# Performance work log

Measured on AMD Instinct MI355X. Metric: run time of the kernel, lower is better.

The kernel has to match this reference:

```python
import jax, jax.numpy as jnp
import numpy as np

EPS = 1e-7  # keras.backend.epsilon()


def setup_inputs() -> dict:
    key = jax.random.key(0)
    k1, k2, k3 = jax.random.split(key, 3)
    B, N, D_in, C, D_out = 32, 2048, 8, 32, 16
    x = jax.random.normal(k1, (B, N, D_in), dtype=jnp.float32)
    W = jax.random.normal(k2, (1, N, C, D_out, D_in), dtype=jnp.float32) * 0.05
    R = jax.random.normal(k3, (1, N, C), dtype=jnp.float32)
    return {"x": x, "W": W, "R": R}


def reference(x, W, R):
    # x: [B, N, D_in]; W: [1, N, C, D_out, D_in]; R: [1, N, C]
    R_nor = jax.nn.softmax(R[0], axis=0)          # softmax over N (axis=1 of [1,N,C])
    # per-capsule transform: u[b,n,c,j] = sum_k W[n,c,j,k] * x[b,n,k]
    u = jnp.einsum('ncjk,bnk->bncj', W[0], x)
    # routing-weighted aggregation over input capsules n
    s = jnp.einsum('bncj,nc->bcj', u, R_nor)      # [B, C, D_out]
    # squash along capsule dim (original axis=-2 before squeeze == D_out)
    ss = jnp.sum(jnp.square(s), axis=-1, keepdims=True) + EPS
    scale = jnp.sqrt(ss) / (1.0 + ss)
    return scale * s                               # [B, C, D_out]
```

## Files before the change

kernel.cpp:

```cpp
#include <hip/hip_runtime.h>
#include <math.h>


#define NN 2048
#define CC 32

__device__ __forceinline__ void g2l16(const float* g, float* l) {
  __builtin_amdgcn_global_load_lds((const __attribute__((address_space(1))) void*)g,
                                   (__attribute__((address_space(3))) void*)l, 16, 0, 0);
}

__global__ void caps_stats(const float* __restrict__ R, float* __restrict__ I) {
  const int c = blockIdx.x;
  const int t = threadIdx.x;
  __shared__ float red[256];
  float s = 0.f;
#pragma unroll
  for (int i = 0; i < 8; ++i) s += expf(R[(size_t)(t + i * 256) * CC + c]);
  red[t] = s;
  __syncthreads();
  for (int h = 128; h >= 1; h >>= 1) {
    if (t < h) red[t] += red[t + h];
    __syncthreads();
  }
  if (t == 0) I[c] = 1.0f / red[0];
}

__global__ void __launch_bounds__(512) caps_main(const float* __restrict__ x,
                                                 const float* __restrict__ W,
                                                 const float* __restrict__ R,
                                                 const float* __restrict__ I,
                                                 float* __restrict__ P) {
  const int bid = blockIdx.x;
  const int cq = bid >> 6;
  const int chunk = bid & 63;
  const int n0 = chunk * 32;
  const int tid = threadIdx.x;
  const int ws = tid >> 6;
  const int lane = tid & 63;
  const int j = lane & 15;
  const int bo = lane >> 4;

  extern __shared__ float smem[];
  float* ldsW = smem;
  float* ldsX = smem + 8192;
  float* wW = ldsW + ws * 1024;
  float* wX = ldsX + ws * 1024;
  const int nw = n0 + ws * 4;

  auto stageW = [&](int nl, int buf) {
#pragma unroll
    for (int i = 0; i < 2; ++i) {
      int S = i * 64 + lane;
      int g = S ^ (((S >> 2) ^ (S >> 4)) & 1) ^ (((S >> 3) & 1) << 1) ^ (((S >> 4) & 1) << 2);
      g2l16(W + (size_t)(nw + nl) * 4096 + cq * 512 + g * 4, wW + buf * 512 + i * 256);
    }
  };
  stageW(0, 0);
  {
    int g2 = lane ^ ((lane >> 4) << 1);
    int b = g2 >> 1, kq = g2 & 1;
    const float* xs = x + (size_t)b * (NN * 8) + kq * 4;
#pragma unroll
    for (int nl = 0; nl < 4; ++nl)
      g2l16(xs + (size_t)(nw + nl) * 8, wX + nl * 256);
  }
  float rv[4][4];
  {
    float4 iv = *(const float4*)(I + cq * 4);
#pragma unroll
    for (int nl = 0; nl < 4; ++nl) {
      float4 rq = *(const float4*)(R + (size_t)(nw + nl) * CC + cq * 4);
      rv[nl][0] = expf(rq.x) * iv.x;
      rv[nl][1] = expf(rq.y) * iv.y;
      rv[nl][2] = expf(rq.z) * iv.z;
      rv[nl][3] = expf(rq.w) * iv.w;
    }
  }

  float acc[4][8];
#pragma unroll
  for (int a = 0; a < 4; ++a)
#pragma unroll
    for (int b = 0; b < 8; ++b) acc[a][b] = 0.f;

  const int jsw = j >> 1;

  auto compute = [&](int nl, int buf) {
    const float* Wn = wW + buf * 512;
    const float* Xn = wX + nl * 256;
#pragma unroll
    for (int kh = 0; kh < 2; ++kh) {
      float4 xv[8];
#pragma unroll
      for (int bi = 0; bi < 8; ++bi) {
        int G = (bo * 8 + bi) * 2 + kh;
        int S = G ^ ((G >> 4) << 1);
        xv[bi] = *(const float4*)(Xn + S * 4);
      }
#pragma unroll
      for (int ci = 0; ci < 4; ++ci) {
        int slot = (ci * 32 + j * 2 + kh) ^ jsw;
        float4 wf = *(const float4*)(Wn + slot * 4);
        float rvv = rv[nl][ci];
        float w0 = wf.x * rvv, w1 = wf.y * rvv, w2 = wf.z * rvv, w3 = wf.w * rvv;
#pragma unroll
        for (int bi = 0; bi < 8; ++bi) {
          float a = acc[ci][bi];
          a = fmaf(w0, xv[bi].x, a);
          a = fmaf(w1, xv[bi].y, a);
          a = fmaf(w2, xv[bi].z, a);
          a = fmaf(w3, xv[bi].w, a);
          acc[ci][bi] = a;
        }
      }
    }
  };

  stageW(1, 1);
  asm volatile("s_waitcnt vmcnt(2)" ::: "memory");
  __builtin_amdgcn_sched_barrier(0);
  compute(0, 0);
  __builtin_amdgcn_sched_barrier(0);
  stageW(2, 0);
  asm volatile("s_waitcnt vmcnt(2)" ::: "memory");
  __builtin_amdgcn_sched_barrier(0);
  compute(1, 1);
  __builtin_amdgcn_sched_barrier(0);
  stageW(3, 1);
  asm volatile("s_waitcnt vmcnt(2)" ::: "memory");
  __builtin_amdgcn_sched_barrier(0);
  compute(2, 0);
  asm volatile("s_waitcnt vmcnt(0)" ::: "memory");
  __builtin_amdgcn_sched_barrier(0);
  compute(3, 1);

#pragma unroll
  for (int ci = 0; ci < 4; ++ci)
#pragma unroll
    for (int bi = 0; bi < 8; ++bi) {
      int cell = (ci * 8 + bi) * 64 + lane;
      float* dst = (ci < 2) ? (ldsW + ws * 1024 + cell)
                            : (ldsX + ws * 1024 + (cell - 1024));
      *dst = acc[ci][bi];
    }
  __syncthreads();
  {
    const int t4 = tid * 4;
    const bool lo = (t4 < 1024);
    float4 ssum = make_float4(0.f, 0.f, 0.f, 0.f);
#pragma unroll
    for (int w = 0; w < 8; ++w) {
      const float* src = lo ? (ldsW + w * 1024 + t4) : (ldsX + w * 1024 + (t4 - 1024));
      float4 v = *(const float4*)src;
      ssum.x += v.x; ssum.y += v.y; ssum.z += v.z; ssum.w += v.w;
    }
    *(float4*)(P + (size_t)bid * 2048 + t4) = ssum;
  }
}

__global__ void caps_reduce(const float* __restrict__ P, float* __restrict__ out) {
  const int g = blockIdx.x * 256 + threadIdx.x;
  const int j = g & 15;
  const int c = (g >> 4) & 31;
  const int b = g >> 9;
  const int bo = b >> 3, bi = b & 7;
  const int cq = c >> 2, ci = c & 3;
  const int idx = (ci * 8 + bi) * 64 + (bo * 16 + j);
  const float* Pq = P + (size_t)cq * 64 * 2048 + idx;

  float s = 0.f;
#pragma unroll 16
  for (int ch = 0; ch < 64; ++ch) {
    s += Pq[(size_t)ch * 2048];
  }
  float sq = s * s;
  sq += __shfl_xor(sq, 8, 16);
  sq += __shfl_xor(sq, 4, 16);
  sq += __shfl_xor(sq, 2, 16);
  sq += __shfl_xor(sq, 1, 16);
  float ss = sq + 1e-7f;
  float scale = sqrtf(ss) / (1.0f + ss);
  out[g] = scale * s;
}

extern "C" void kernel_launch(void* const* d_in, const int* in_sizes, int n_in,
                              void* d_out, int out_size, void* d_ws, size_t ws_size,
                              hipStream_t stream) {
  const float* x = (const float*)d_in[0];
  const float* W = (const float*)d_in[1];
  const float* R = (const float*)d_in[2];
  float* out = (float*)d_out;

  float* I = (float*)d_ws;
  float* P = (float*)d_ws + 64;

  hipFuncSetAttribute((const void*)caps_main,
                      hipFuncAttributeMaxDynamicSharedMemorySize, 65536);

  caps_stats<<<32, 256, 0, stream>>>(R, I);
  caps_main<<<512, 512, 65536, stream>>>(x, W, R, I, P);
  caps_reduce<<<64, 256, 0, stream>>>(P, out);
}
```

Measured before the change: 26.93 us.

## Process eight capsules per block with triple-buffered W staging

Each block now handles eight output capsules instead of four, which halves the grid to 256 blocks and doubles the per-thread accumulator tile so x values loaded from LDS are reused across more capsules. W staging moves to three LDS buffers with deeper prefetch and adjusted waitcnts, and the R loads are hoisted ahead of the staging. LDS per block grows to 128KB and register pressure roughly doubles, which risks lower occupancy and fewer blocks than CUs.

```diff
diff --git a/kernel.cpp b/kernel.cpp
--- a/kernel.cpp
+++ b/kernel.cpp
@@ -32,7 +32,7 @@
                                                  const float* __restrict__ I,
                                                  float* __restrict__ P) {
   const int bid = blockIdx.x;
-  const int cq = bid >> 6;
+  const int cg = bid >> 6;
   const int chunk = bid & 63;
   const int n0 = chunk * 32;
   const int tid = threadIdx.x;
@@ -42,20 +42,30 @@
   const int bo = lane >> 4;
 
   extern __shared__ float smem[];
-  float* ldsW = smem;
-  float* ldsX = smem + 8192;
-  float* wW = ldsW + ws * 1024;
-  float* wX = ldsX + ws * 1024;
+  float* wREG = smem + ws * 4096;
+  float* wW = wREG;
+  float* wX = wREG + 3072;
   const int nw = n0 + ws * 4;
 
+  float4 iv0 = *(const float4*)(I + cg * 8);
+  float4 iv1 = *(const float4*)(I + cg * 8 + 4);
+  float4 rq0[4], rq1[4];
+#pragma unroll
+  for (int nl = 0; nl < 4; ++nl) {
+    rq0[nl] = *(const float4*)(R + (size_t)(nw + nl) * CC + cg * 8);
+    rq1[nl] = *(const float4*)(R + (size_t)(nw + nl) * CC + cg * 8 + 4);
+  }
+
   auto stageW = [&](int nl, int buf) {
 #pragma unroll
-    for (int i = 0; i < 2; ++i) {
+    for (int i = 0; i < 4; ++i) {
       int S = i * 64 + lane;
-      int g = S ^ (((S >> 2) ^ (S >> 4)) & 1) ^ (((S >> 3) & 1) << 1) ^ (((S >> 4) & 1) << 2);
-      g2l16(W + (size_t)(nw + nl) * 4096 + cq * 512 + g * 4, wW + buf * 512 + i * 256);
+      int g = S ^ ((S >> 3) & 3);
+      g2l16(W + (size_t)(nw + nl) * 4096 + cg * 1024 + g * 4,
+            wW + buf * 1024 + i * 256);
     }
   };
+
   stageW(0, 0);
   {
     int g2 = lane ^ ((lane >> 4) << 1);
@@ -65,29 +75,29 @@
     for (int nl = 0; nl < 4; ++nl)
       g2l16(xs + (size_t)(nw + nl) * 8, wX + nl * 256);
   }
-  float rv[4][4];
-  {
-    float4 iv = *(const float4*)(I + cq * 4);
-#pragma unroll
-    for (int nl = 0; nl < 4; ++nl) {
-      float4 rq = *(const float4*)(R + (size_t)(nw + nl) * CC + cq * 4);
-      rv[nl][0] = expf(rq.x) * iv.x;
-      rv[nl][1] = expf(rq.y) * iv.y;
-      rv[nl][2] = expf(rq.z) * iv.z;
-      rv[nl][3] = expf(rq.w) * iv.w;
-    }
-  }
-
-  float acc[4][8];
-#pragma unroll
-  for (int a = 0; a < 4; ++a)
+  stageW(1, 1);
+
+  float rv[4][8];
+#pragma unroll
+  for (int nl = 0; nl < 4; ++nl) {
+    rv[nl][0] = expf(rq0[nl].x) * iv0.x;
+    rv[nl][1] = expf(rq0[nl].y) * iv0.y;
+    rv[nl][2] = expf(rq0[nl].z) * iv0.z;
+    rv[nl][3] = expf(rq0[nl].w) * iv0.w;
+    rv[nl][4] = expf(rq1[nl].x) * iv1.x;
+    rv[nl][5] = expf(rq1[nl].y) * iv1.y;
+    rv[nl][6] = expf(rq1[nl].z) * iv1.z;
+    rv[nl][7] = expf(rq1[nl].w) * iv1.w;
+  }
+
+  float acc[8][8];
+#pragma unroll
+  for (int a = 0; a < 8; ++a)
 #pragma unroll
     for (int b = 0; b < 8; ++b) acc[a][b] = 0.f;
 
-  const int jsw = j >> 1;
-
   auto compute = [&](int nl, int buf) {
-    const float* Wn = wW + buf * 512;
+    const float* Wn = wW + buf * 1024;
     const float* Xn = wX + nl * 256;
 #pragma unroll
     for (int kh = 0; kh < 2; ++kh) {
@@ -99,8 +109,8 @@
         xv[bi] = *(const float4*)(Xn + S * 4);
       }
 #pragma unroll
-      for (int ci = 0; ci < 4; ++ci) {
-        int slot = (ci * 32 + j * 2 + kh) ^ jsw;
+      for (int ci = 0; ci < 8; ++ci) {
+        int slot = (ci * 32 + j * 2 + kh) ^ (j >> 2);
         float4 wf = *(const float4*)(Wn + slot * 4);
         float rvv = rv[nl][ci];
         float w0 = wf.x * rvv, w1 = wf.y * rvv, w2 = wf.z * rvv, w3 = wf.w * rvv;
@@ -117,45 +127,41 @@
     }
   };
 
-  stageW(1, 1);
-  asm volatile("s_waitcnt vmcnt(2)" ::: "memory");
+  stageW(2, 2);
+  asm volatile("s_waitcnt vmcnt(8)" ::: "memory");
   __builtin_amdgcn_sched_barrier(0);
   compute(0, 0);
-  __builtin_amdgcn_sched_barrier(0);
-  stageW(2, 0);
-  asm volatile("s_waitcnt vmcnt(2)" ::: "memory");
+  asm volatile("s_waitcnt lgkmcnt(0)" ::: "memory");
+  __builtin_amdgcn_sched_barrier(0);
+  stageW(3, 0);
+  asm volatile("s_waitcnt vmcnt(8)" ::: "memory");
   __builtin_amdgcn_sched_barrier(0);
   compute(1, 1);
-  __builtin_amdgcn_sched_barrier(0);
-  stageW(3, 1);
-  asm volatile("s_waitcnt vmcnt(2)" ::: "memory");
-  __builtin_amdgcn_sched_barrier(0);
-  compute(2, 0);
+  asm volatile("s_waitcnt vmcnt(4)" ::: "memory");
+  __builtin_amdgcn_sched_barrier(0);
+  compute(2, 2);
   asm volatile("s_waitcnt vmcnt(0)" ::: "memory");
   __builtin_amdgcn_sched_barrier(0);
-  compute(3, 1);
-
-#pragma unroll
-  for (int ci = 0; ci < 4; ++ci)
-#pragma unroll
-    for (int bi = 0; bi < 8; ++bi) {
-      int cell = (ci * 8 + bi) * 64 + lane;
-      float* dst = (ci < 2) ? (ldsW + ws * 1024 + cell)
-                            : (ldsX + ws * 1024 + (cell - 1024));
-      *dst = acc[ci][bi];
-    }
+  compute(3, 0);
+
+#pragma unroll
+  for (int ci = 0; ci < 8; ++ci)
+#pragma unroll
+    for (int bi = 0; bi < 8; ++bi)
+      wREG[(ci * 8 + bi) * 64 + lane] = acc[ci][bi];
   __syncthreads();
   {
-    const int t4 = tid * 4;
-    const bool lo = (t4 < 1024);
-    float4 ssum = make_float4(0.f, 0.f, 0.f, 0.f);
-#pragma unroll
-    for (int w = 0; w < 8; ++w) {
-      const float* src = lo ? (ldsW + w * 1024 + t4) : (ldsX + w * 1024 + (t4 - 1024));
-      float4 v = *(const float4*)src;
-      ssum.x += v.x; ssum.y += v.y; ssum.z += v.z; ssum.w += v.w;
-    }
-    *(float4*)(P + (size_t)bid * 2048 + t4) = ssum;
+    float ssum[8];
+#pragma unroll
+    for (int i = 0; i < 8; ++i) ssum[i] = 0.f;
+#pragma unroll
+    for (int w = 0; w < 8; ++w)
+#pragma unroll
+      for (int i = 0; i < 8; ++i)
+        ssum[i] += smem[(size_t)w * 4096 + (ws * 8 + i) * 64 + lane];
+#pragma unroll
+    for (int i = 0; i < 8; ++i)
+      P[(size_t)bid * 4096 + (ws * 8 + i) * 64 + lane] = ssum[i];
   }
 }
 
@@ -165,14 +171,14 @@
   const int c = (g >> 4) & 31;
   const int b = g >> 9;
   const int bo = b >> 3, bi = b & 7;
-  const int cq = c >> 2, ci = c & 3;
+  const int cg = c >> 3, ci = c & 7;
   const int idx = (ci * 8 + bi) * 64 + (bo * 16 + j);
-  const float* Pq = P + (size_t)cq * 64 * 2048 + idx;
+  const float* Pq = P + (size_t)cg * 64 * 4096 + idx;
 
   float s = 0.f;
 #pragma unroll 16
   for (int ch = 0; ch < 64; ++ch) {
-    s += Pq[(size_t)ch * 2048];
+    s += Pq[(size_t)ch * 4096];
   }
   float sq = s * s;
   sq += __shfl_xor(sq, 8, 16);
@@ -196,9 +202,9 @@
   float* P = (float*)d_ws + 64;
 
   hipFuncSetAttribute((const void*)caps_main,
-                      hipFuncAttributeMaxDynamicSharedMemorySize, 65536);
+                      hipFuncAttributeMaxDynamicSharedMemorySize, 131072);
 
   caps_stats<<<32, 256, 0, stream>>>(R, I);
-  caps_main<<<512, 512, 65536, stream>>>(x, W, R, I, P);
+  caps_main<<<256, 512, 131072, stream>>>(x, W, R, I, P);
   caps_reduce<<<64, 256, 0, stream>>>(P, out);
 }
```

Result: slower. 28.68 us (+6.5%).

## Defer softmax normalization to reduce kernel, drop separate stats launch

Applied to the files above, without the earlier changes.

Removes the caps_stats kernel and stops multiplying by the softmax denominator in the main kernel. Because the denominator is constant per capsule c, it is factored out of the sum over n. Each reduce block now recomputes the column sums of exp(R) for its 16 capsules and scales the partial sums before the squash. It also moves the R loads and the second W stage earlier to overlap them with the exp computation. This trades one kernel launch and a dependency for redundant exp work in every reduce block (64 blocks each reading 16 columns of R), and that extra work lengthens the reduce kernel.

```diff
diff --git a/kernel.cpp b/kernel.cpp
--- a/kernel.cpp
+++ b/kernel.cpp
@@ -10,26 +10,9 @@
                                    (__attribute__((address_space(3))) void*)l, 16, 0, 0);
 }
 
-__global__ void caps_stats(const float* __restrict__ R, float* __restrict__ I) {
-  const int c = blockIdx.x;
-  const int t = threadIdx.x;
-  __shared__ float red[256];
-  float s = 0.f;
-#pragma unroll
-  for (int i = 0; i < 8; ++i) s += expf(R[(size_t)(t + i * 256) * CC + c]);
-  red[t] = s;
-  __syncthreads();
-  for (int h = 128; h >= 1; h >>= 1) {
-    if (t < h) red[t] += red[t + h];
-    __syncthreads();
-  }
-  if (t == 0) I[c] = 1.0f / red[0];
-}
-
 __global__ void __launch_bounds__(512) caps_main(const float* __restrict__ x,
                                                  const float* __restrict__ W,
                                                  const float* __restrict__ R,
-                                                 const float* __restrict__ I,
                                                  float* __restrict__ P) {
   const int bid = blockIdx.x;
   const int cq = bid >> 6;
@@ -48,6 +31,11 @@
   float* wX = ldsX + ws * 1024;
   const int nw = n0 + ws * 4;
 
+  float4 rq[4];
+#pragma unroll
+  for (int nl = 0; nl < 4; ++nl)
+    rq[nl] = *(const float4*)(R + (size_t)(nw + nl) * CC + cq * 4);
+
   auto stageW = [&](int nl, int buf) {
 #pragma unroll
     for (int i = 0; i < 2; ++i) {
@@ -56,6 +44,7 @@
       g2l16(W + (size_t)(nw + nl) * 4096 + cq * 512 + g * 4, wW + buf * 512 + i * 256);
     }
   };
+
   stageW(0, 0);
   {
     int g2 = lane ^ ((lane >> 4) << 1);
@@ -65,17 +54,15 @@
     for (int nl = 0; nl < 4; ++nl)
       g2l16(xs + (size_t)(nw + nl) * 8, wX + nl * 256);
   }
+  stageW(1, 1);
+
   float rv[4][4];
-  {
-    float4 iv = *(const float4*)(I + cq * 4);
-#pragma unroll
-    for (int nl = 0; nl < 4; ++nl) {
-      float4 rq = *(const float4*)(R + (size_t)(nw + nl) * CC + cq * 4);
-      rv[nl][0] = expf(rq.x) * iv.x;
-      rv[nl][1] = expf(rq.y) * iv.y;
-      rv[nl][2] = expf(rq.z) * iv.z;
-      rv[nl][3] = expf(rq.w) * iv.w;
-    }
+#pragma unroll
+  for (int nl = 0; nl < 4; ++nl) {
+    rv[nl][0] = expf(rq[nl].x);
+    rv[nl][1] = expf(rq[nl].y);
+    rv[nl][2] = expf(rq[nl].z);
+    rv[nl][3] = expf(rq[nl].w);
   }
 
   float acc[4][8];
@@ -117,7 +104,6 @@
     }
   };
 
-  stageW(1, 1);
   asm volatile("s_waitcnt vmcnt(2)" ::: "memory");
   __builtin_amdgcn_sched_barrier(0);
   compute(0, 0);
@@ -159,8 +145,32 @@
   }
 }
 
-__global__ void caps_reduce(const float* __restrict__ P, float* __restrict__ out) {
-  const int g = blockIdx.x * 256 + threadIdx.x;
+__global__ void caps_reduce(const float* __restrict__ P, const float* __restrict__ R,
+                            float* __restrict__ out) {
+  const int t = threadIdx.x;
+  const int bid = blockIdx.x;
+
+  __shared__ float red[256];
+  __shared__ float invd[16];
+  {
+    const int cl = t & 15, nf = t >> 4;
+    const int c0 = (bid * 16) & 31;
+    float s = 0.f;
+#pragma unroll 16
+    for (int i = 0; i < 128; ++i)
+      s += expf(R[(size_t)(nf + i * 16) * CC + c0 + cl]);
+    red[t] = s;
+  }
+  __syncthreads();
+#pragma unroll
+  for (int h = 8; h >= 1; h >>= 1) {
+    if ((t >> 4) < h) red[t] += red[t + h * 16];
+    __syncthreads();
+  }
+  if (t < 16) invd[t] = 1.0f / red[t];
+  __syncthreads();
+
+  const int g = bid * 256 + t;
   const int j = g & 15;
   const int c = (g >> 4) & 31;
   const int b = g >> 9;
@@ -171,9 +181,10 @@
 
   float s = 0.f;
 #pragma unroll 16
-  for (int ch = 0; ch < 64; ++ch) {
+  for (int ch = 0; ch < 64; ++ch)
     s += Pq[(size_t)ch * 2048];
-  }
+  s *= invd[t >> 4];
+
   float sq = s * s;
   sq += __shfl_xor(sq, 8, 16);
   sq += __shfl_xor(sq, 4, 16);
@@ -191,14 +202,11 @@
   const float* W = (const float*)d_in[1];
   const float* R = (const float*)d_in[2];
   float* out = (float*)d_out;
-
-  float* I = (float*)d_ws;
-  float* P = (float*)d_ws + 64;
+  float* P = (float*)d_ws;
 
   hipFuncSetAttribute((const void*)caps_main,
                       hipFuncAttributeMaxDynamicSharedMemorySize, 65536);
 
-  caps_stats<<<32, 256, 0, stream>>>(R, I);
-  caps_main<<<512, 512, 65536, stream>>>(x, W, R, I, P);
-  caps_reduce<<<64, 256, 0, stream>>>(P, out);
-}
+  caps_main<<<512, 512, 65536, stream>>>(x, W, R, P);
+  caps_reduce<<<64, 256, 0, stream>>>(P, R, out);
+}
```

Measured after the change: 28.39 us. 1.05x slower.
